# Kernel tuning notes

Hardware: AMD Instinct MI355X
Metric: run time of the kernel (lower is better)

The kernel has to match this reference:

```python
import jax, jax.numpy as jnp
import numpy as np

N, E, D, H, F = 50000, 800000, 256, 4, 32
NEG_SLOPE = 0.2

def setup_inputs() -> dict:
    key = jax.random.key(0)
    ks = jax.random.split(key, 8)
    h = jax.random.normal(ks[0], (N, D), dtype=jnp.float32)
    W = jax.random.normal(ks[1], (D, H * F), dtype=jnp.float32) * (1.0 / np.sqrt(D))
    attn_l_w = jax.random.normal(ks[2], (F, 1), dtype=jnp.float32) * (1.0 / np.sqrt(F))
    attn_l_b = jnp.zeros((1,), dtype=jnp.float32)
    attn_r_w = jax.random.normal(ks[3], (F, 1), dtype=jnp.float32) * (1.0 / np.sqrt(F))
    attn_r_b = jnp.zeros((1,), dtype=jnp.float32)
    bias = jnp.zeros((H, F), dtype=jnp.float32)
    src = jax.random.randint(ks[4], (E,), 0, N, dtype=jnp.int32)
    dst = jax.random.randint(ks[5], (E,), 0, N, dtype=jnp.int32)
    return {"h": h, "W": W, "attn_l_w": attn_l_w, "attn_l_b": attn_l_b,
            "attn_r_w": attn_r_w, "attn_r_b": attn_r_b, "bias": bias,
            "src": src, "dst": dst}

def reference(h, W, attn_l_w, attn_l_b, attn_r_w, attn_r_b, bias, src, dst):
    # node projection: [N, D] @ [D, H*F] -> [N, H, F]
    hW = (h @ W).reshape(N, H, F)
    # per-node attention halves: Dense(1) over F -> [N, H, 1]
    el = jnp.einsum('nhf,fo->nho', hW, attn_l_w) + attn_l_b
    er = jnp.einsum('nhf,fo->nho', hW, attn_r_w) + attn_r_b
    # edge logits: src contributes er, dst contributes el -> [E, H, 1]
    e = er[src] + el[dst]
    e = jnp.where(e >= 0, e, NEG_SLOPE * e)  # leaky_relu
    # segment softmax over destination groups
    emax = jax.ops.segment_max(e, dst, num_segments=N)  # [N, H, 1]
    ee = jnp.exp(e - emax[dst])
    denom = jax.ops.segment_sum(ee, dst, num_segments=N)  # [N, H, 1]
    a = ee / denom[dst]  # [E, H, 1]
    # weighted message scatter-sum: [E, H, F] -> [N, H, F]
    m = hW[src] * a
    out = jax.ops.segment_sum(m, dst, num_segments=N) + bias
    return out
```

## Files before the change

kernel.cpp:

```cpp
#include <hip/hip_runtime.h>
#include <hip/hip_bf16.h>

#define N_NODES 50000
#define E_EDGES 800000
#define D_IN    256
#define H_HEADS 4
#define HF      128
#define NEG_SLOPE 0.2f
#define SCAN_BLOCKS ((N_NODES + 255) / 256)
#define HIST_BLOCKS (E_EDGES / 256)
#define PREP_BLOCKS 128
#define FILL_PASSES 8
#define NODES_PER_PASS (N_NODES / FILL_PASSES)

typedef __attribute__((ext_vector_type(8))) short bf16x8;
typedef __attribute__((ext_vector_type(4))) float f32x4;

__global__ __launch_bounds__(256) void k_hist_prep(const int* __restrict__ dst,
                                                   unsigned* __restrict__ cnt,
                                                   const float* __restrict__ W,
                                                   __hip_bfloat16* __restrict__ Wt) {
    const int b = blockIdx.x;
    if (b < HIST_BLOCKS) {
        const int g = b * 256 + threadIdx.x;
        atomicAdd(&cnt[dst[g]], 1u);
    } else {
        const int g = (b - HIST_BLOCKS) * 256 + threadIdx.x;
        const int n = g >> 8;
        const int k = g & 255;
        Wt[n * D_IN + k] = __float2bfloat16(W[k * HF + n]);
    }
}

__global__ __launch_bounds__(256) void k_scan(const unsigned* __restrict__ cnt,
                                              unsigned* __restrict__ off) {
    __shared__ unsigned s[256];
    const int t = threadIdx.x;
    const int b = blockIdx.x;
    const int base = b * 256;

    unsigned part = 0;
    #pragma unroll 4
    for (int i = t; i < base; i += 256) part += cnt[i];
    s[t] = part;
    __syncthreads();
    #pragma unroll
    for (int o = 128; o > 0; o >>= 1) {
        if (t < o) s[t] += s[t + o];
        __syncthreads();
    }
    const unsigned pre = s[0];
    __syncthreads();

    const int g = base + t;
    const unsigned x = (g < N_NODES) ? cnt[g] : 0u;
    s[t] = x;
    __syncthreads();
    unsigned inc = x;
    #pragma unroll
    for (int o = 1; o < 256; o <<= 1) {
        const unsigned v = (t >= o) ? s[t - o] : 0u;
        __syncthreads();
        inc += v;
        s[t] = inc;
        __syncthreads();
    }
    if (g < N_NODES) off[g] = pre + inc - x;
}

__global__ __launch_bounds__(256) void k_fill(const int* __restrict__ src,
                                              const int* __restrict__ dst,
                                              unsigned* __restrict__ off,
                                              unsigned* __restrict__ perm) {
    const int pass  = blockIdx.x / HIST_BLOCKS;
    const int chunk = blockIdx.x - pass * HIST_BLOCKS;
    const int g = chunk * 256 + threadIdx.x;
    const int d = dst[g];
    const int lo = pass * NODES_PER_PASS;
    if ((unsigned)(d - lo) < (unsigned)NODES_PER_PASS) {
        const unsigned p = atomicAdd(&off[d], 1u);
        perm[p] = (unsigned)src[g];
    }
}

__global__ __launch_bounds__(256) void k_gemm(const float* __restrict__ h,
                                              const __hip_bfloat16* __restrict__ Wt,
                                              const float* __restrict__ lw,
                                              const float* __restrict__ lb,
                                              const float* __restrict__ rw,
                                              const float* __restrict__ rb,
                                              __hip_bfloat16* __restrict__ hW,
                                              float* __restrict__ el,
                                              float* __restrict__ er) {
    __shared__ __hip_bfloat16 As[64][72];
    __shared__ __hip_bfloat16 Bs[128][72];
    const int t    = threadIdx.x;
    const int r0   = blockIdx.x * 64;
    const int wave = t >> 6;
    const int lane = t & 63;
    const int l16  = lane & 15;
    const int quad = lane >> 4;

    f32x4 acc[8] = {};

    for (int k0 = 0; k0 < D_IN; k0 += 64) {
        {
            const int row  = t >> 2;
            const int koff = (t & 3) * 16;
            const int n    = r0 + row;
            float v[16];
            if (n < N_NODES) {
                const float* p = h + (size_t)n * D_IN + k0 + koff;
                *(float4*)&v[0]  = ((const float4*)p)[0];
                *(float4*)&v[4]  = ((const float4*)p)[1];
                *(float4*)&v[8]  = ((const float4*)p)[2];
                *(float4*)&v[12] = ((const float4*)p)[3];
            } else {
                #pragma unroll
                for (int i = 0; i < 16; ++i) v[i] = 0.f;
            }
            __hip_bfloat16 b[16];
            #pragma unroll
            for (int i = 0; i < 16; ++i) b[i] = __float2bfloat16(v[i]);
            *(uint4*)&As[row][koff]     = ((uint4*)b)[0];
            *(uint4*)&As[row][koff + 8] = ((uint4*)b)[1];
        }
        {
            const int n    = t >> 1;
            const int koff = (t & 1) * 32;
            const uint4* p = (const uint4*)(Wt + n * D_IN + k0 + koff);
            uint4 b0 = p[0], b1 = p[1], b2 = p[2], b3 = p[3];
            uint4* q = (uint4*)&Bs[n][koff];
            q[0] = b0; q[1] = b1; q[2] = b2; q[3] = b3;
        }
        __syncthreads();

        #pragma unroll
        for (int ks = 0; ks < 2; ++ks) {
            const bf16x8 af = *(const bf16x8*)&As[wave * 16 + l16][ks * 32 + quad * 8];
            #pragma unroll
            for (int nt = 0; nt < 8; ++nt) {
                const bf16x8 bfg = *(const bf16x8*)&Bs[nt * 16 + l16][ks * 32 + quad * 8];
                acc[nt] = __builtin_amdgcn_mfma_f32_16x16x32_bf16(af, bfg, acc[nt], 0, 0, 0);
            }
        }
        __syncthreads();
    }

    const int mbase = r0 + wave * 16 + quad * 4;
    #pragma unroll
    for (int nt = 0; nt < 8; ++nt) {
        #pragma unroll
        for (int r = 0; r < 4; ++r) {
            const int m = mbase + r;
            if (m < N_NODES)
                hW[(size_t)m * HF + nt * 16 + l16] = __float2bfloat16(acc[nt][r]);
        }
    }

    const float lwv0 = lw[l16], lwv1 = lw[l16 + 16];
    const float rwv0 = rw[l16], rwv1 = rw[l16 + 16];
    const float lb0 = lb[0], rb0 = rb[0];
    #pragma unroll
    for (int r = 0; r < 4; ++r) {
        const int m = mbase + r;
        float el4[4], er4[4];
        #pragma unroll
        for (int hh = 0; hh < 4; ++hh) {
            float pl = acc[2 * hh][r] * lwv0 + acc[2 * hh + 1][r] * lwv1;
            float pr = acc[2 * hh][r] * rwv0 + acc[2 * hh + 1][r] * rwv1;
            #pragma unroll
            for (int o = 1; o < 16; o <<= 1) {
                pl += __shfl_xor(pl, o);
                pr += __shfl_xor(pr, o);
            }
            el4[hh] = pl + lb0;
            er4[hh] = pr + rb0;
        }
        if (l16 == 0 && m < N_NODES) {
            *(float4*)&el[m * H_HEADS] = make_float4(el4[0], el4[1], el4[2], el4[3]);
            *(float4*)&er[m * H_HEADS] = make_float4(er4[0], er4[1], er4[2], er4[3]);
        }
    }
}

__global__ __launch_bounds__(256) void k_aggregate(const __hip_bfloat16* __restrict__ hW,
                                                   const float* __restrict__ el,
                                                   const float* __restrict__ er,
                                                   const unsigned* __restrict__ off_end,
                                                   const unsigned* __restrict__ perm,
                                                   const float* __restrict__ bias,
                                                   float* __restrict__ out) {
    const int wave = threadIdx.x >> 6;
    const int lane = threadIdx.x & 63;
    const int n    = blockIdx.x * 4 + wave;
    const int hh   = lane >> 4;
    const unsigned beg = (n == 0) ? 0u : off_end[n - 1];
    const unsigned end = off_end[n];
    const float eld = el[n * H_HEADS + hh];
    const unsigned* hWu = (const unsigned*)hW;

    float a0 = 0.f, a1 = 0.f, denom = 0.f;
    unsigned j = beg;
    for (; j + 4 <= end; j += 4) {
        int s[4];
        #pragma unroll
        for (int u = 0; u < 4; ++u) s[u] = (int)perm[j + u];
        unsigned g2[4];
        float e4[4];
        #pragma unroll
        for (int u = 0; u < 4; ++u) {
            g2[u] = hWu[(size_t)s[u] * (HF / 2) + lane];
            e4[u] = er[s[u] * H_HEADS + hh];
        }
        #pragma unroll
        for (int u = 0; u < 4; ++u) {
            float v = e4[u] + eld;
            v = (v >= 0.f) ? v : NEG_SLOPE * v;
            const float p = __expf(v);
            denom += p;
            a0 += p * __uint_as_float(g2[u] << 16);
            a1 += p * __uint_as_float(g2[u] & 0xFFFF0000u);
        }
    }
    for (; j < end; ++j) {
        const int si = (int)perm[j];
        const unsigned g2 = hWu[(size_t)si * (HF / 2) + lane];
        float v = er[si * H_HEADS + hh] + eld;
        v = (v >= 0.f) ? v : NEG_SLOPE * v;
        const float p = __expf(v);
        denom += p;
        a0 += p * __uint_as_float(g2 << 16);
        a1 += p * __uint_as_float(g2 & 0xFFFF0000u);
    }
    const float inv = (end > beg) ? 1.f / denom : 0.f;
    const float2 bv = *(const float2*)&bias[lane * 2];
    float2 o2 = make_float2(a0 * inv + bv.x, a1 * inv + bv.y);
    *(float2*)&out[(size_t)n * HF + lane * 2] = o2;
}

extern "C" void kernel_launch(void* const* d_in, const int* in_sizes, int n_in,
                              void* d_out, int out_size, void* d_ws, size_t ws_size,
                              hipStream_t stream) {
    const float* h    = (const float*)d_in[0];
    const float* W    = (const float*)d_in[1];
    const float* lw   = (const float*)d_in[2];
    const float* lb   = (const float*)d_in[3];
    const float* rw   = (const float*)d_in[4];
    const float* rb   = (const float*)d_in[5];
    const float* bias = (const float*)d_in[6];
    const int*   src  = (const int*)d_in[7];
    const int*   dst  = (const int*)d_in[8];
    float* out = (float*)d_out;

    float*    ws   = (float*)d_ws;
    float*    el   = ws;
    float*    er   = ws + 200000;
    unsigned* cnt  = (unsigned*)(ws + 400000);
    unsigned* off  = (unsigned*)(ws + 450000);
    unsigned* perm = (unsigned*)(ws + 500000);
    __hip_bfloat16* Wt = (__hip_bfloat16*)(ws + 1300000);
    __hip_bfloat16* hW = (__hip_bfloat16*)(ws + 1320000);

    hipMemsetAsync(cnt, 0, N_NODES * sizeof(unsigned), stream);
    k_hist_prep<<<HIST_BLOCKS + PREP_BLOCKS, 256, 0, stream>>>(dst, cnt, W, Wt);
    k_scan<<<SCAN_BLOCKS, 256, 0, stream>>>(cnt, off);
    k_fill<<<FILL_PASSES * HIST_BLOCKS, 256, 0, stream>>>(src, dst, off, perm);
    k_gemm<<<(N_NODES + 63) / 64, 256, 0, stream>>>(h, Wt, lw, lb, rw, rb, hW, el, er);
    k_aggregate<<<N_NODES / 4, 256, 0, stream>>>(hW, el, er, off, perm, bias, out);
}
```

Before: 249.2 us.

## Fuse histogram into GEMM launch, replace memset, split aggregation wave by edge halves

Memset is replaced by zeroing blocks inside the weight-transpose kernel. The dst histogram atomics now run as extra blocks of the GEMM launch, so histogram and projection can overlap and one launch is dropped. The aggregation kernel now has each half-wave process a different edge with 8-byte hW loads, then combines the two halves with a cross-lane shuffle. This doubles edge-level memory parallelism per wave, at the cost of idle lanes on odd tails and a reduction step.

Result: faster. 229.2 us (-8.0%).

```diff
diff --git a/kernel.cpp b/kernel.cpp
--- a/kernel.cpp
+++ b/kernel.cpp
@@ -10,90 +10,52 @@
 #define SCAN_BLOCKS ((N_NODES + 255) / 256)
 #define HIST_BLOCKS (E_EDGES / 256)
 #define PREP_BLOCKS 128
+#define ZERO_BLOCKS SCAN_BLOCKS
+#define GEMM_BLOCKS ((N_NODES + 63) / 64)
 #define FILL_PASSES 8
 #define NODES_PER_PASS (N_NODES / FILL_PASSES)
 
 typedef __attribute__((ext_vector_type(8))) short bf16x8;
 typedef __attribute__((ext_vector_type(4))) float f32x4;
 
-__global__ __launch_bounds__(256) void k_hist_prep(const int* __restrict__ dst,
-                                                   unsigned* __restrict__ cnt,
+__device__ __forceinline__ float bf_lo(unsigned u) { return __uint_as_float(u << 16); }
+__device__ __forceinline__ float bf_hi(unsigned u) { return __uint_as_float(u & 0xFFFF0000u); }
+
+__global__ __launch_bounds__(256) void k_zero_prep(unsigned* __restrict__ cnt,
                                                    const float* __restrict__ W,
                                                    __hip_bfloat16* __restrict__ Wt) {
     const int b = blockIdx.x;
-    if (b < HIST_BLOCKS) {
+    if (b < ZERO_BLOCKS) {
         const int g = b * 256 + threadIdx.x;
-        atomicAdd(&cnt[dst[g]], 1u);
+        if (g < N_NODES) cnt[g] = 0u;
     } else {
-        const int g = (b - HIST_BLOCKS) * 256 + threadIdx.x;
+        const int g = (b - ZERO_BLOCKS) * 256 + threadIdx.x;
         const int n = g >> 8;
         const int k = g & 255;
         Wt[n * D_IN + k] = __float2bfloat16(W[k * HF + n]);
     }
 }
 
-__global__ __launch_bounds__(256) void k_scan(const unsigned* __restrict__ cnt,
-                                              unsigned* __restrict__ off) {
-    __shared__ unsigned s[256];
-    const int t = threadIdx.x;
-    const int b = blockIdx.x;
-    const int base = b * 256;
-
-    unsigned part = 0;
-    #pragma unroll 4
-    for (int i = t; i < base; i += 256) part += cnt[i];
-    s[t] = part;
-    __syncthreads();
-    #pragma unroll
-    for (int o = 128; o > 0; o >>= 1) {
-        if (t < o) s[t] += s[t + o];
-        __syncthreads();
-    }
-    const unsigned pre = s[0];
-    __syncthreads();
-
-    const int g = base + t;
-    const unsigned x = (g < N_NODES) ? cnt[g] : 0u;
-    s[t] = x;
-    __syncthreads();
-    unsigned inc = x;
-    #pragma unroll
-    for (int o = 1; o < 256; o <<= 1) {
-        const unsigned v = (t >= o) ? s[t - o] : 0u;
-        __syncthreads();
-        inc += v;
-        s[t] = inc;
-        __syncthreads();
-    }
-    if (g < N_NODES) off[g] = pre + inc - x;
-}
-
-__global__ __launch_bounds__(256) void k_fill(const int* __restrict__ src,
-                                              const int* __restrict__ dst,
-                                              unsigned* __restrict__ off,
-                                              unsigned* __restrict__ perm) {
-    const int pass  = blockIdx.x / HIST_BLOCKS;
-    const int chunk = blockIdx.x - pass * HIST_BLOCKS;
-    const int g = chunk * 256 + threadIdx.x;
-    const int d = dst[g];
-    const int lo = pass * NODES_PER_PASS;
-    if ((unsigned)(d - lo) < (unsigned)NODES_PER_PASS) {
-        const unsigned p = atomicAdd(&off[d], 1u);
-        perm[p] = (unsigned)src[g];
-    }
-}
-
-__global__ __launch_bounds__(256) void k_gemm(const float* __restrict__ h,
-                                              const __hip_bfloat16* __restrict__ Wt,
-                                              const float* __restrict__ lw,
-                                              const float* __restrict__ lb,
-                                              const float* __restrict__ rw,
-                                              const float* __restrict__ rb,
-                                              __hip_bfloat16* __restrict__ hW,
-                                              float* __restrict__ el,
-                                              float* __restrict__ er) {
+__global__ __launch_bounds__(256) void k_gemm_hist(const float* __restrict__ h,
+                                                   const __hip_bfloat16* __restrict__ Wt,
+                                                   const float* __restrict__ lw,
+                                                   const float* __restrict__ lb,
+                                                   const float* __restrict__ rw,
+                                                   const float* __restrict__ rb,
+                                                   __hip_bfloat16* __restrict__ hW,
+                                                   float* __restrict__ el,
+                                                   float* __restrict__ er,
+                                                   const int* __restrict__ dst,
+                                                   unsigned* __restrict__ cnt) {
     __shared__ __hip_bfloat16 As[64][72];
     __shared__ __hip_bfloat16 Bs[128][72];
+
+    if (blockIdx.x >= GEMM_BLOCKS) {
+        const int g = (blockIdx.x - GEMM_BLOCKS) * 256 + threadIdx.x;
+        atomicAdd(&cnt[dst[g]], 1u);
+        return;
+    }
+
     const int t    = threadIdx.x;
     const int r0   = blockIdx.x * 64;
     const int wave = t >> 6;
@@ -184,6 +146,57 @@
     }
 }
 
+__global__ __launch_bounds__(256) void k_scan(const unsigned* __restrict__ cnt,
+                                              unsigned* __restrict__ off) {
+    __shared__ unsigned s[256];
+    const int t = threadIdx.x;
+    const int b = blockIdx.x;
+    const int base = b * 256;
+
+    unsigned part = 0;
+    #pragma unroll 4
+    for (int i = t; i < base; i += 256) part += cnt[i];
+    s[t] = part;
+    __syncthreads();
+    #pragma unroll
+    for (int o = 128; o > 0; o >>= 1) {
+        if (t < o) s[t] += s[t + o];
+        __syncthreads();
+    }
+    const unsigned pre = s[0];
+    __syncthreads();
+
+    const int g = base + t;
+    const unsigned x = (g < N_NODES) ? cnt[g] : 0u;
+    s[t] = x;
+    __syncthreads();
+    unsigned inc = x;
+    #pragma unroll
+    for (int o = 1; o < 256; o <<= 1) {
+        const unsigned v = (t >= o) ? s[t - o] : 0u;
+        __syncthreads();
+        inc += v;
+        s[t] = inc;
+        __syncthreads();
+    }
+    if (g < N_NODES) off[g] = pre + inc - x;
+}
+
+__global__ __launch_bounds__(256) void k_fill(const int* __restrict__ src,
+                                              const int* __restrict__ dst,
+                                              unsigned* __restrict__ off,
+                                              unsigned* __restrict__ perm) {
+    const int pass  = blockIdx.x / HIST_BLOCKS;
+    const int chunk = blockIdx.x - pass * HIST_BLOCKS;
+    const int g = chunk * 256 + threadIdx.x;
+    const int d = dst[g];
+    const int lo = pass * NODES_PER_PASS;
+    if ((unsigned)(d - lo) < (unsigned)NODES_PER_PASS) {
+        const unsigned p = atomicAdd(&off[d], 1u);
+        perm[p] = (unsigned)src[g];
+    }
+}
+
 __global__ __launch_bounds__(256) void k_aggregate(const __hip_bfloat16* __restrict__ hW,
                                                    const float* __restrict__ el,
                                                    const float* __restrict__ er,
@@ -193,50 +206,60 @@
                                                    float* __restrict__ out) {
     const int wave = threadIdx.x >> 6;
     const int lane = threadIdx.x & 63;
+    const int half = lane >> 5;
+    const int l    = lane & 31;
+    const int hh   = l >> 3;
     const int n    = blockIdx.x * 4 + wave;
-    const int hh   = lane >> 4;
     const unsigned beg = (n == 0) ? 0u : off_end[n - 1];
     const unsigned end = off_end[n];
-    const float eld = el[n * H_HEADS + hh];
-    const unsigned* hWu = (const unsigned*)hW;
-
-    float a0 = 0.f, a1 = 0.f, denom = 0.f;
+    const float eld = el[(unsigned)n * H_HEADS + hh];
+    const uint2* hW2 = (const uint2*)hW;
+
+    float a0 = 0.f, a1 = 0.f, a2 = 0.f, a3 = 0.f, denom = 0.f;
     unsigned j = beg;
     for (; j + 4 <= end; j += 4) {
-        int s[4];
-        #pragma unroll
-        for (int u = 0; u < 4; ++u) s[u] = (int)perm[j + u];
-        unsigned g2[4];
-        float e4[4];
-        #pragma unroll
-        for (int u = 0; u < 4; ++u) {
-            g2[u] = hWu[(size_t)s[u] * (HF / 2) + lane];
-            e4[u] = er[s[u] * H_HEADS + hh];
-        }
-        #pragma unroll
-        for (int u = 0; u < 4; ++u) {
-            float v = e4[u] + eld;
-            v = (v >= 0.f) ? v : NEG_SLOPE * v;
-            const float p = __expf(v);
-            denom += p;
-            a0 += p * __uint_as_float(g2[u] << 16);
-            a1 += p * __uint_as_float(g2[u] & 0xFFFF0000u);
-        }
-    }
-    for (; j < end; ++j) {
-        const int si = (int)perm[j];
-        const unsigned g2 = hWu[(size_t)si * (HF / 2) + lane];
-        float v = er[si * H_HEADS + hh] + eld;
-        v = (v >= 0.f) ? v : NEG_SLOPE * v;
-        const float p = __expf(v);
+        const unsigned s0 = perm[j + half];
+        const unsigned s1 = perm[j + 2 + half];
+        const float er0 = er[s0 * H_HEADS + hh];
+        const float er1 = er[s1 * H_HEADS + hh];
+        const uint2 g0 = hW2[s0 * 32u + l];
+        const uint2 g1 = hW2[s1 * 32u + l];
+        float v0 = er0 + eld; v0 = (v0 >= 0.f) ? v0 : NEG_SLOPE * v0;
+        float v1 = er1 + eld; v1 = (v1 >= 0.f) ? v1 : NEG_SLOPE * v1;
+        const float p0 = __expf(v0);
+        const float p1 = __expf(v1);
+        denom += p0 + p1;
+        a0 += p0 * bf_lo(g0.x) + p1 * bf_lo(g1.x);
+        a1 += p0 * bf_hi(g0.x) + p1 * bf_hi(g1.x);
+        a2 += p0 * bf_lo(g0.y) + p1 * bf_lo(g1.y);
+        a3 += p0 * bf_hi(g0.y) + p1 * bf_hi(g1.y);
+    }
+    for (; j < end; j += 2) {
+        const unsigned i = j + half;
+        const bool ok = (i < end);
+        const unsigned s = ok ? perm[i] : 0u;
+        const float erv = er[s * H_HEADS + hh];
+        const uint2 g = hW2[s * 32u + l];
+        float v = erv + eld; v = (v >= 0.f) ? v : NEG_SLOPE * v;
+        const float p = ok ? __expf(v) : 0.f;
         denom += p;
-        a0 += p * __uint_as_float(g2 << 16);
-        a1 += p * __uint_as_float(g2 & 0xFFFF0000u);
-    }
-    const float inv = (end > beg) ? 1.f / denom : 0.f;
-    const float2 bv = *(const float2*)&bias[lane * 2];
-    float2 o2 = make_float2(a0 * inv + bv.x, a1 * inv + bv.y);
-    *(float2*)&out[(size_t)n * HF + lane * 2] = o2;
+        a0 += p * bf_lo(g.x);
+        a1 += p * bf_hi(g.x);
+        a2 += p * bf_lo(g.y);
+        a3 += p * bf_hi(g.y);
+    }
+    denom += __shfl_xor(denom, 32);
+    a0 += __shfl_xor(a0, 32);
+    a1 += __shfl_xor(a1, 32);
+    a2 += __shfl_xor(a2, 32);
+    a3 += __shfl_xor(a3, 32);
+    if (half == 0) {
+        const float inv = (end > beg) ? 1.f / denom : 0.f;
+        const float4 bv = *(const float4*)&bias[l * 4];
+        float4 o = make_float4(a0 * inv + bv.x, a1 * inv + bv.y,
+                               a2 * inv + bv.z, a3 * inv + bv.w);
+        *(float4*)&out[(unsigned)n * HF + l * 4] = o;
+    }
 }
 
 extern "C" void kernel_launch(void* const* d_in, const int* in_sizes, int n_in,
@@ -262,10 +285,10 @@
     __hip_bfloat16* Wt = (__hip_bfloat16*)(ws + 1300000);
     __hip_bfloat16* hW = (__hip_bfloat16*)(ws + 1320000);
 
-    hipMemsetAsync(cnt, 0, N_NODES * sizeof(unsigned), stream);
-    k_hist_prep<<<HIST_BLOCKS + PREP_BLOCKS, 256, 0, stream>>>(dst, cnt, W, Wt);
+    k_zero_prep<<<ZERO_BLOCKS + PREP_BLOCKS, 256, 0, stream>>>(cnt, W, Wt);
+    k_gemm_hist<<<GEMM_BLOCKS + HIST_BLOCKS, 256, 0, stream>>>(
+        h, Wt, lw, lb, rw, rb, hW, el, er, dst, cnt);
     k_scan<<<SCAN_BLOCKS, 256, 0, stream>>>(cnt, off);
     k_fill<<<FILL_PASSES * HIST_BLOCKS, 256, 0, stream>>>(src, dst, off, perm);
-    k_gemm<<<(N_NODES + 63) / 64, 256, 0, stream>>>(h, Wt, lw, lb, rw, rb, hW, el, er);
     k_aggregate<<<N_NODES / 4, 256, 0, stream>>>(hW, el, er, off, perm, bias, out);
 }
```
